# Optimization experiments

Measured on AMD Instinct MI355X. Metric: run time of the kernel, lower is better.

Reference implementation:

```python
import jax, jax.numpy as jnp
import numpy as np

H = 125      # LSTM hidden per direction
MLP = 100    # hidden_MLP
N = 1024     # sentence length


def _lstm_dir(x, wih, whh, bih, bhh, reverse):
    # x: [n, din]; torch gate order i, f, g, o
    b = bih + bhh
    def step(carry, xt):
        h, c = carry
        g = xt @ wih.T + h @ whh.T + b
        i, f, gg, o = jnp.split(g, 4)
        c = jax.nn.sigmoid(f) * c + jax.nn.sigmoid(i) * jnp.tanh(gg)
        h = jax.nn.sigmoid(o) * jnp.tanh(c)
        return (h, c), h
    z = jnp.zeros((H,), x.dtype)
    _, hs = jax.lax.scan(step, (z, z), x, reverse=reverse)
    return hs  # [n, H]


def _bilstm(x, pf, pb):
    return jnp.concatenate([_lstm_dir(x, *pf, reverse=False),
                            _lstm_dir(x, *pb, reverse=True)], axis=-1)


def setup_inputs() -> dict:
    key = jax.random.key(0)
    ks = iter(jax.random.split(key, 32))
    p = lambda shape, s=0.1: jax.random.normal(next(ks), shape, jnp.float32) * s
    inp = {}
    inp["word_idx"] = jax.random.randint(next(ks), (1, N), 0, 15948)
    inp["pos_idx"] = jax.random.randint(next(ks), (1, N), 0, 47)
    inp["true_tree_heads"] = jax.random.randint(next(ks), (N,), 0, N)
    inp["word_emb"] = p((15948, 100), 1.0)
    inp["pos_emb"] = p((47, 25), 1.0)
    for l, din in ((0, 125), (1, 250)):
        for d in ("f", "b"):
            inp[f"w_ih_{l}{d}"] = p((4 * H, din))
            inp[f"w_hh_{l}{d}"] = p((4 * H, H))
            inp[f"b_ih_{l}{d}"] = p((4 * H,))
            inp[f"b_hh_{l}{d}"] = p((4 * H,))
    inp["w1"] = p((MLP, 2 * H)); inp["b1"] = p((MLP,))
    inp["w2"] = p((MLP, 2 * H)); inp["b2"] = p((MLP,))
    inp["w3"] = p((MLP,)); inp["b3"] = p(())
    return inp


def reference(word_idx, pos_idx, true_tree_heads, word_emb, pos_emb,
              w_ih_0f, w_hh_0f, b_ih_0f, b_hh_0f,
              w_ih_0b, w_hh_0b, b_ih_0b, b_hh_0b,
              w_ih_1f, w_hh_1f, b_ih_1f, b_hh_1f,
              w_ih_1b, w_hh_1b, b_ih_1b, b_hh_1b,
              w1, b1, w2, b2, w3, b3):
    # embeddings: [n, 125]
    emb = jnp.concatenate([word_emb[word_idx[0]], pos_emb[pos_idx[0]]], axis=-1)
    h0 = _bilstm(emb, (w_ih_0f, w_hh_0f, b_ih_0f, b_hh_0f),
                 (w_ih_0b, w_hh_0b, b_ih_0b, b_hh_0b))            # [n, 250]
    h1 = _bilstm(h0, (w_ih_1f, w_hh_1f, b_ih_1f, b_hh_1f),
                 (w_ih_1b, w_hh_1b, b_ih_1b, b_hh_1b))            # [n, 250]
    heads = h1 @ w1.T + b1   # [n, 100]
    mods = h1 @ w2.T + b2    # [n, 100]
    # tag_scores[h, m] = layer3(tanh(heads[h] + mods[m])), diagonal = -inf
    s = jnp.tanh(heads[:, None, :] + mods[None, :, :])            # [n, n, 100]
    scores = jnp.einsum('hmd,d->hm', s, w3) + b3
    n = scores.shape[0]
    return jnp.where(jnp.eye(n, dtype=bool), -jnp.inf, scores)
```

## Files before the change

kernel.cpp:

```cpp
#include <hip/hip_runtime.h>
#include <hip/hip_bf16.h>

#define H 125
#define G4 500
#define NN 1024
#define DMLP 100

#define SCL1 (-1.4426950408889634f)
#define SCL2 (-2.8853900817779268f)

typedef __attribute__((ext_vector_type(4))) float f32x4;
typedef __attribute__((ext_vector_type(4))) int   i32x4;
typedef __attribute__((ext_vector_type(8))) int   i32x8;

__device__ __forceinline__ float frcp(float x) { return __builtin_amdgcn_rcpf(x); }
__device__ __forceinline__ float fexp2(float x) {
    float r;
    asm("v_exp_f32 %0, %1" : "=v"(r) : "v"(x));
    return r;
}

__device__ __forceinline__ float bf16_quant(float v) {
    return __bfloat162float(__float2bfloat16(v));
}

__global__ __launch_bounds__(512) void ingemm4a_k(
    const int* __restrict__ wid, const int* __restrict__ pid,
    const float* __restrict__ wemb, const float* __restrict__ pemb,
    const float* __restrict__ wf, const float* __restrict__ bif, const float* __restrict__ bhf,
    const float* __restrict__ wb, const float* __restrict__ bib, const float* __restrict__ bhb,
    float* __restrict__ xg4f, float* __restrict__ xg4b)
{
    __shared__ float xs[8][125];
    const int dir = blockIdx.y;
    const float* __restrict__ w  = dir ? wb  : wf;
    const float* __restrict__ bi = dir ? bib : bif;
    const float* __restrict__ bh = dir ? bhb : bhf;
    float* __restrict__ xg       = dir ? xg4b : xg4f;

    const int t0  = blockIdx.x * 8;
    const int tid = threadIdx.x;
    for (int i = tid; i < 8 * 125; i += 512) {
        int r = i / 125, k = i - r * 125;
        int t = t0 + r;
        xs[r][k] = (k < 100) ? wemb[wid[t] * 100 + k] : pemb[pid[t] * 25 + (k - 100)];
    }
    __syncthreads();

    if (tid < G4) {
        const int g = tid / 125;
        const int u = tid - g * 125;
        const float sg = (g == 2) ? SCL2 : SCL1;
        const float* wr = w + tid * 125;
        float base = bi[tid] + bh[tid];
        float acc[8];
#pragma unroll
        for (int tt = 0; tt < 8; ++tt) acc[tt] = base;
        for (int k = 0; k < 125; ++k) {
            float wv = wr[k];
#pragma unroll
            for (int tt = 0; tt < 8; ++tt) acc[tt] += wv * xs[tt][k];
        }
#pragma unroll
        for (int tt = 0; tt < 8; ++tt) xg[(t0 + tt) * 512 + u * 4 + g] = acc[tt] * sg;
    } else {
        const int qq = tid - G4;
#pragma unroll
        for (int tt = 0; tt < 8; ++tt) xg[(t0 + tt) * 512 + G4 + qq] = 0.f;
    }
}

__global__ __launch_bounds__(512) void ingemm4_k(
    const float* __restrict__ x,
    const float* __restrict__ wf, const float* __restrict__ bif, const float* __restrict__ bhf,
    const float* __restrict__ wb, const float* __restrict__ bib, const float* __restrict__ bhb,
    float* __restrict__ xg4f, float* __restrict__ xg4b)
{
    __shared__ float xs[8][250];
    const int dir = blockIdx.y;
    const float* __restrict__ w  = dir ? wb  : wf;
    const float* __restrict__ bi = dir ? bib : bif;
    const float* __restrict__ bh = dir ? bhb : bhf;
    float* __restrict__ xg       = dir ? xg4b : xg4f;

    const int t0  = blockIdx.x * 8;
    const int tid = threadIdx.x;
    for (int i = tid; i < 8 * 250; i += 512) {
        int r = i / 250;
        xs[r][i - r * 250] = x[t0 * 250 + i];
    }
    __syncthreads();

    if (tid < G4) {
        const int g = tid / 125;
        const int u = tid - g * 125;
        const float sg = (g == 2) ? SCL2 : SCL1;
        const float* wr = w + tid * 250;
        float base = bi[tid] + bh[tid];
        float acc[8];
#pragma unroll
        for (int tt = 0; tt < 8; ++tt) acc[tt] = base;
        for (int k = 0; k < 250; ++k) {
            float wv = wr[k];
#pragma unroll
            for (int tt = 0; tt < 8; ++tt) acc[tt] += wv * xs[tt][k];
        }
#pragma unroll
        for (int tt = 0; tt < 8; ++tt) xg[(t0 + tt) * 512 + u * 4 + g] = acc[tt] * sg;
    } else {
        const int qq = tid - G4;
#pragma unroll
        for (int tt = 0; tt < 8; ++tt) xg[(t0 + tt) * 512 + G4 + qq] = 0.f;
    }
}

__global__ __launch_bounds__(64) void whhprep8_k(
    const float* __restrict__ whh_f, const float* __restrict__ whh_b,
    int* __restrict__ out)
{
    const int dir = blockIdx.y;
    const float* __restrict__ whh = dir ? whh_b : whh_f;
    const int tg = blockIdx.x;
    const int l  = threadIdx.x;
    const int R  = tg * 16 + (l & 15);
    const int u  = R >> 2, g = R & 3;
    const float sg = (g == 2) ? SCL2 : SCL1;
    const int kb = (l >> 4) * 32;
    float f[32];
#pragma unroll
    for (int e = 0; e < 32; ++e) {
        const int k = kb + e;
        f[e] = (u < H && k < H) ? whh[(g * H + u) * H + k] * sg : 0.f;
    }
    int* dst = out + ((dir * 32 + tg) * 64 + l) * 8;
#pragma unroll
    for (int j = 0; j < 8; ++j) {
        int lo = __builtin_amdgcn_cvt_pk_fp8_f32(f[4 * j + 0], f[4 * j + 1], 0,  false);
        int wv = __builtin_amdgcn_cvt_pk_fp8_f32(f[4 * j + 2], f[4 * j + 3], lo, true);
        dst[j] = wv;
    }
}

__global__ __launch_bounds__(1024, 1) void lstm_scan9_k(
    const float* __restrict__ xg_f, const float* __restrict__ xg_b,
    const int* __restrict__ whhA,
    float* __restrict__ hout)
{
    __shared__ __align__(16) unsigned char hb8[128];
    __shared__ __align__(16) float gates[128 * 4];
    const int dir = blockIdx.x;
    const float* __restrict__ xg = dir ? xg_b : xg_f;
    const int col = dir ? H : 0;

    const int tid = threadIdx.x;
    const int w = tid >> 6;
    const int l = tid & 63;
    const int q = l >> 4;
    const int c = l & 15;

    const i32x8* Ab = (const i32x8*)whhA;
    i32x8 A0 = Ab[(dir * 32 + w * 2 + 0) * 64 + l];
    i32x8 A1 = Ab[(dir * 32 + w * 2 + 1) * 64 + l];

    if (tid < 128) hb8[tid] = 0;
    __syncthreads();

    const int usel = 8 * w + 4 * (c & 1) + q;
    const bool writer = (c < 2);
    const int xoff = 32 * w + 16 * (c & 1) + 4 * q;

    float cst = 0.f;
    auto T = [&](int s) { return dir ? (NN - 1 - s) : s; };

    auto LOADX = [&](int s_) -> f32x4 {
        const int sc = (s_ < NN) ? s_ : NN - 1;
        return *(const f32x4*)(xg + T(sc) * 512 + xoff);
    };

    auto STEP = [&](int t, f32x4 x) {
        i32x8 B = *(const i32x8*)(hb8 + 32 * q);
        f32x4 a0 = __builtin_amdgcn_mfma_scale_f32_16x16x128_f8f6f4(
            A0, B, x, 0, 0, 0, 0x7F7F7F7F, 0, 0x7F7F7F7F);
        f32x4 a1 = __builtin_amdgcn_mfma_scale_f32_16x16x128_f8f6f4(
            A1, B, x, 0, 0, 0, 0x7F7F7F7F, 0, 0x7F7F7F7F);
        if (writer) {
            f32x4 gv = (c & 1) ? a1 : a0;
            *(f32x4*)(gates + 4 * usel) = gv;
        }
        asm volatile("s_waitcnt lgkmcnt(0)" ::: "memory");
        __builtin_amdgcn_s_barrier();
        __builtin_amdgcn_sched_barrier(0);
        if (tid < 128) {
            f32x4 g = *(const f32x4*)(gates + 4 * tid);
            const float ai = frcp(1.f + fexp2(g.x));
            const float af = frcp(1.f + fexp2(g.y));
            const float ag = 2.f * frcp(1.f + fexp2(g.z)) - 1.f;
            const float ao = frcp(1.f + fexp2(g.w));
            cst = af * cst + ai * ag;
            const float th = 2.f * frcp(1.f + fexp2(cst * SCL2)) - 1.f;
            const float hv = ao * th;
            int pk = __builtin_amdgcn_cvt_pk_fp8_f32(hv, 0.f, 0, false);
            hb8[tid] = (unsigned char)(pk & 0xFF);
            if (tid < H) hout[t * 250 + col + tid] = hv;
        }
        asm volatile("s_waitcnt lgkmcnt(0)" ::: "memory");
        __builtin_amdgcn_s_barrier();
        __builtin_amdgcn_sched_barrier(0);
    };

    f32x4 p0 = LOADX(0), p1 = LOADX(1);
#pragma unroll 1
    for (int s = 0; s < NN; s += 4) {
        f32x4 n0 = LOADX(s + 2), n1 = LOADX(s + 3);
        STEP(T(s),     p0);
        STEP(T(s + 1), p1);
        p0 = LOADX(s + 4); p1 = LOADX(s + 5);
        STEP(T(s + 2), n0);
        STEP(T(s + 3), n1);
    }
}

__global__ __launch_bounds__(256) void headmod_k(
    const float* __restrict__ h1,
    const float* __restrict__ w1, const float* __restrict__ b1,
    const float* __restrict__ w2, const float* __restrict__ b2,
    float* __restrict__ heads, float* __restrict__ mods)
{
    __shared__ float xs[8][250];
    const int t0  = blockIdx.x * 8;
    const int tid = threadIdx.x;
    for (int i = tid; i < 8 * 250; i += 256) {
        int r = i / 250;
        xs[r][i - r * 250] = h1[t0 * 250 + i];
    }
    __syncthreads();

    int d; const float* w; float bb; float* o;
    if (tid < DMLP)                          { d = tid;       w = w1 + d * 250; bb = b1[d]; o = heads; }
    else if (tid >= 128 && tid < 128 + DMLP) { d = tid - 128; w = w2 + d * 250; bb = b2[d]; o = mods;  }
    else return;

    float acc[8];
#pragma unroll
    for (int tt = 0; tt < 8; ++tt) acc[tt] = bb;
    for (int k = 0; k < 250; ++k) {
        float wv = w[k];
#pragma unroll
        for (int tt = 0; tt < 8; ++tt) acc[tt] += wv * xs[tt][k];
    }
#pragma unroll
    for (int tt = 0; tt < 8; ++tt) o[(t0 + tt) * DMLP + d] = acc[tt];
}

__global__ __launch_bounds__(256) void scores_k(
    const float* __restrict__ heads, const float* __restrict__ mods,
    const float* __restrict__ w3, const float* __restrict__ b3,
    float* __restrict__ out)
{
    __shared__ __align__(16) float hh[16][DMLP];
    __shared__ __align__(16) float mm[16][DMLP];
    __shared__ __align__(16) float ws3[DMLP];
    const int bh = blockIdx.y * 16, bm = blockIdx.x * 16;
    const int tid = threadIdx.x;
    for (int i = tid; i < 16 * DMLP; i += 256) {
        int r = i / DMLP, d = i - r * DMLP;
        hh[r][d] = heads[(bh + r) * DMLP + d];
        mm[r][d] = mods[(bm + r) * DMLP + d];
    }
    if (tid < DMLP) ws3[tid] = w3[tid];
    __syncthreads();

    const int tx = tid & 15, ty = tid >> 4;
    const f32x4* h4 = (const f32x4*)hh[ty];
    const f32x4* m4 = (const f32x4*)mm[tx];
    const f32x4* w4 = (const f32x4*)ws3;
    float acc = 0.f;
#pragma unroll
    for (int qq = 0; qq < DMLP / 4; ++qq) {
        f32x4 v  = h4[qq] + m4[qq];
        f32x4 wv = w4[qq];
#pragma unroll
        for (int e = 0; e < 4; ++e) {
            float th = 2.f * frcp(1.f + fexp2(v[e] * SCL2)) - 1.f;
            acc += wv[e] * th;
        }
    }
    acc += b3[0];
    const int hrow = bh + ty, mcol = bm + tx;
    float v = (hrow == mcol) ? -3.3895313892515355e38f : bf16_quant(acc);
    out[hrow * NN + mcol] = v;
}

extern "C" void kernel_launch(void* const* d_in, const int* in_sizes, int n_in,
                              void* d_out, int out_size, void* d_ws, size_t ws_size,
                              hipStream_t stream)
{
    const int*   wid   = (const int*)d_in[0];
    const int*   pid   = (const int*)d_in[1];
    const float* wemb  = (const float*)d_in[3];
    const float* pemb  = (const float*)d_in[4];
    const float* wih0f = (const float*)d_in[5];
    const float* whh0f = (const float*)d_in[6];
    const float* bih0f = (const float*)d_in[7];
    const float* bhh0f = (const float*)d_in[8];
    const float* wih0b = (const float*)d_in[9];
    const float* whh0b = (const float*)d_in[10];
    const float* bih0b = (const float*)d_in[11];
    const float* bhh0b = (const float*)d_in[12];
    const float* wih1f = (const float*)d_in[13];
    const float* whh1f = (const float*)d_in[14];
    const float* bih1f = (const float*)d_in[15];
    const float* bhh1f = (const float*)d_in[16];
    const float* wih1b = (const float*)d_in[17];
    const float* whh1b = (const float*)d_in[18];
    const float* bih1b = (const float*)d_in[19];
    const float* bhh1b = (const float*)d_in[20];
    const float* w1    = (const float*)d_in[21];
    const float* b1    = (const float*)d_in[22];
    const float* w2    = (const float*)d_in[23];
    const float* b2    = (const float*)d_in[24];
    const float* w3    = (const float*)d_in[25];
    const float* b3    = (const float*)d_in[26];

    float* ws    = (float*)d_ws;
    float* xgf   = ws;
    float* xgb   = ws + 524288;
    float* h0    = ws + 1048576;
    float* h1    = ws + 1304576;
    float* hd    = ws + 1560576;
    float* md    = ws + 1662976;
    int*   whhA0 = (int*)(ws + 1765376);
    int*   whhA1 = (int*)(ws + 1798144);

    whhprep8_k<<<dim3(32, 2), 64, 0, stream>>>(whh0f, whh0b, whhA0);
    whhprep8_k<<<dim3(32, 2), 64, 0, stream>>>(whh1f, whh1b, whhA1);

    ingemm4a_k<<<dim3(NN / 8, 2), 512, 0, stream>>>(
        wid, pid, wemb, pemb,
        wih0f, bih0f, bhh0f, wih0b, bih0b, bhh0b, xgf, xgb);

    lstm_scan9_k<<<2, 1024, 0, stream>>>(xgf, xgb, whhA0, h0);

    ingemm4_k<<<dim3(NN / 8, 2), 512, 0, stream>>>(
        h0, wih1f, bih1f, bhh1f, wih1b, bih1b, bhh1b, xgf, xgb);

    lstm_scan9_k<<<2, 1024, 0, stream>>>(xgf, xgb, whhA1, h1);

    headmod_k<<<NN / 8, 256, 0, stream>>>(h1, w1, b1, w2, b2, hd, md);

    scores_k<<<dim3(NN / 16, NN / 16), 256, 0, stream>>>(hd, md, w3, b3, (float*)d_out);
}
```

Measured before the change: 1.032 ms.

## Halve LSTM scan block to 8 waves with four MFMAs per wave

The recurrent LSTM scan kernel now runs with 512 threads instead of 1024, each wave issuing four scaled FP8 MFMAs instead of two, so fewer waves take part in the two barriers per timestep. The gate-writer mapping and x offsets are adjusted to match. The elementwise cell update gets setprio for its threads and is rewritten with FMAs. The two weight-prep launches are merged into one grid with a layer dimension to save a launch. The cost is more serial MFMA work per wave on the critical path of each step.

Result: faster. 1.004 ms (-2.8%).

```diff
diff --git a/kernel.cpp b/kernel.cpp
--- a/kernel.cpp
+++ b/kernel.cpp
@@ -115,11 +115,14 @@
 }
 
 __global__ __launch_bounds__(64) void whhprep8_k(
-    const float* __restrict__ whh_f, const float* __restrict__ whh_b,
-    int* __restrict__ out)
-{
+    const float* __restrict__ w0f, const float* __restrict__ w0b,
+    const float* __restrict__ w1f, const float* __restrict__ w1b,
+    int* __restrict__ out0, int* __restrict__ out1)
+{
+    const int lay = blockIdx.z;
     const int dir = blockIdx.y;
-    const float* __restrict__ whh = dir ? whh_b : whh_f;
+    const float* __restrict__ whh = lay ? (dir ? w1b : w1f) : (dir ? w0b : w0f);
+    int* __restrict__ out = lay ? out1 : out0;
     const int tg = blockIdx.x;
     const int l  = threadIdx.x;
     const int R  = tg * 16 + (l & 15);
@@ -141,7 +144,7 @@
     }
 }
 
-__global__ __launch_bounds__(1024, 1) void lstm_scan9_k(
+__global__ __launch_bounds__(512, 1) void lstm_scan10_k(
     const float* __restrict__ xg_f, const float* __restrict__ xg_b,
     const int* __restrict__ whhA,
     float* __restrict__ hout)
@@ -159,15 +162,18 @@
     const int c = l & 15;
 
     const i32x8* Ab = (const i32x8*)whhA;
-    i32x8 A0 = Ab[(dir * 32 + w * 2 + 0) * 64 + l];
-    i32x8 A1 = Ab[(dir * 32 + w * 2 + 1) * 64 + l];
+    i32x8 A0 = Ab[(dir * 32 + w * 4 + 0) * 64 + l];
+    i32x8 A1 = Ab[(dir * 32 + w * 4 + 1) * 64 + l];
+    i32x8 A2 = Ab[(dir * 32 + w * 4 + 2) * 64 + l];
+    i32x8 A3 = Ab[(dir * 32 + w * 4 + 3) * 64 + l];
 
     if (tid < 128) hb8[tid] = 0;
     __syncthreads();
-
-    const int usel = 8 * w + 4 * (c & 1) + q;
-    const bool writer = (c < 2);
-    const int xoff = 32 * w + 16 * (c & 1) + 4 * q;
+    if (tid < 128) __builtin_amdgcn_s_setprio(1);
+
+    const int usel = 16 * w + 4 * (c & 3) + q;
+    const bool writer = (c < 4);
+    const int xoff = 4 * usel;
 
     float cst = 0.f;
     auto T = [&](int s) { return dir ? (NN - 1 - s) : s; };
@@ -183,8 +189,14 @@
             A0, B, x, 0, 0, 0, 0x7F7F7F7F, 0, 0x7F7F7F7F);
         f32x4 a1 = __builtin_amdgcn_mfma_scale_f32_16x16x128_f8f6f4(
             A1, B, x, 0, 0, 0, 0x7F7F7F7F, 0, 0x7F7F7F7F);
+        f32x4 a2 = __builtin_amdgcn_mfma_scale_f32_16x16x128_f8f6f4(
+            A2, B, x, 0, 0, 0, 0x7F7F7F7F, 0, 0x7F7F7F7F);
+        f32x4 a3 = __builtin_amdgcn_mfma_scale_f32_16x16x128_f8f6f4(
+            A3, B, x, 0, 0, 0, 0x7F7F7F7F, 0, 0x7F7F7F7F);
         if (writer) {
-            f32x4 gv = (c & 1) ? a1 : a0;
+            f32x4 s0 = (c & 1) ? a1 : a0;
+            f32x4 s1 = (c & 1) ? a3 : a2;
+            f32x4 gv = (c & 2) ? s1 : s0;
             *(f32x4*)(gates + 4 * usel) = gv;
         }
         asm volatile("s_waitcnt lgkmcnt(0)" ::: "memory");
@@ -194,11 +206,12 @@
             f32x4 g = *(const f32x4*)(gates + 4 * tid);
             const float ai = frcp(1.f + fexp2(g.x));
             const float af = frcp(1.f + fexp2(g.y));
-            const float ag = 2.f * frcp(1.f + fexp2(g.z)) - 1.f;
+            const float sgm = frcp(1.f + fexp2(g.z));
             const float ao = frcp(1.f + fexp2(g.w));
-            cst = af * cst + ai * ag;
-            const float th = 2.f * frcp(1.f + fexp2(cst * SCL2)) - 1.f;
-            const float hv = ao * th;
+            const float ag = __builtin_fmaf(2.f, sgm, -1.f);
+            cst = __builtin_fmaf(af, cst, ai * ag);
+            const float r = frcp(1.f + fexp2(cst * SCL2));
+            const float hv = __builtin_fmaf(2.f * ao, r, -ao);
             int pk = __builtin_amdgcn_cvt_pk_fp8_f32(hv, 0.f, 0, false);
             hb8[tid] = (unsigned char)(pk & 0xFF);
             if (tid < H) hout[t * 250 + col + tid] = hv;
@@ -332,19 +345,19 @@
     int*   whhA0 = (int*)(ws + 1765376);
     int*   whhA1 = (int*)(ws + 1798144);
 
-    whhprep8_k<<<dim3(32, 2), 64, 0, stream>>>(whh0f, whh0b, whhA0);
-    whhprep8_k<<<dim3(32, 2), 64, 0, stream>>>(whh1f, whh1b, whhA1);
+    whhprep8_k<<<dim3(32, 2, 2), 64, 0, stream>>>(
+        whh0f, whh0b, whh1f, whh1b, whhA0, whhA1);
 
     ingemm4a_k<<<dim3(NN / 8, 2), 512, 0, stream>>>(
         wid, pid, wemb, pemb,
         wih0f, bih0f, bhh0f, wih0b, bih0b, bhh0b, xgf, xgb);
 
-    lstm_scan9_k<<<2, 1024, 0, stream>>>(xgf, xgb, whhA0, h0);
+    lstm_scan10_k<<<2, 512, 0, stream>>>(xgf, xgb, whhA0, h0);
 
     ingemm4_k<<<dim3(NN / 8, 2), 512, 0, stream>>>(
         h0, wih1f, bih1f, bhh1f, wih1b, bih1b, bhh1b, xgf, xgb);
 
-    lstm_scan9_k<<<2, 1024, 0, stream>>>(xgf, xgb, whhA1, h1);
+    lstm_scan10_k<<<2, 512, 0, stream>>>(xgf, xgb, whhA1, h1);
 
     headmod_k<<<NN / 8, 256, 0, stream>>>(h1, w1, b1, w2, b2, hd, md);
 
```
